# Optimization experiments

Measured on AMD Instinct MI355X. Metric: run time of the kernel, lower is better.

## Reference

```python
import jax, jax.numpy as jnp
import numpy as np

N_NODES = 100000
N_RELS = 237
N_EDGES = 500000
D_IN = 128
D_HID = 128
D_OUT = 128


def setup_inputs() -> dict:
    key = jax.random.key(0)
    ks = jax.random.split(key, 13)
    src = jax.random.randint(ks[0], (N_EDGES,), 0, N_NODES, dtype=jnp.int32)
    dst = jax.random.randint(ks[1], (N_EDGES,), 0, N_NODES, dtype=jnp.int32)
    rel = jax.random.randint(ks[2], (N_EDGES,), 0, N_RELS, dtype=jnp.int32)
    triplets = jnp.stack([src, dst, rel], axis=1)  # [E, 3]
    s = 0.05
    return {
        "triplets": triplets,
        "ent_embed": jax.random.normal(ks[3], (N_NODES, D_IN), jnp.float32) * s,
        "rel_embed": jax.random.normal(ks[4], (N_RELS, D_IN), jnp.float32) * s,
        "W_ent": jax.random.normal(ks[5], (D_IN, D_HID), jnp.float32) * s,
        "b_ent": jnp.zeros((D_HID,), jnp.float32),
        "W_rel": jax.random.normal(ks[6], (D_IN, D_HID), jnp.float32) * s,
        "b_rel": jnp.zeros((D_HID,), jnp.float32),
        "W_ent2": jax.random.normal(ks[7], (3 * D_HID, D_OUT), jnp.float32) * s,
        "b_ent2": jnp.zeros((D_OUT,), jnp.float32),
        "a_w": jax.random.normal(ks[8], (D_OUT, 1), jnp.float32) * s,
        "a_b": jnp.zeros((1,), jnp.float32),
    }


def reference(triplets, ent_embed, rel_embed, W_ent, b_ent, W_rel, b_rel,
              W_ent2, b_ent2, a_w, a_b):
    src_i, dst_i, rel_i = triplets[:, 0], triplets[:, 1], triplets[:, 2]
    # embedding gathers
    src = ent_embed[src_i]          # [E, D_IN]
    dst = ent_embed[dst_i]          # [E, D_IN]
    rel = rel_embed[rel_i]          # [E, D_IN]
    # shared fc_ent projection on src and dst, fc_rel on rel
    src = src @ W_ent + b_ent       # [E, D_HID]
    dst = dst @ W_ent + b_ent
    rel = rel @ W_rel + b_rel
    # per-edge feature c = fc_ent2(cat([src, dst, rel]))
    c = jnp.concatenate([src, dst, rel], axis=1) @ W_ent2 + b_ent2  # [E, D_OUT]
    # unnormalized exp attention score (leaky_relu slope 0.01, torch default)
    b = jnp.exp(jax.nn.leaky_relu((c @ a_w + a_b)[:, 0], negative_slope=0.01))  # [E]
    # segment softmax over edges sharing a source node
    b_sum = jax.ops.segment_sum(b, src_i, num_segments=N_NODES)  # [N]
    alpha = b / b_sum[src_i]                                     # [E]
    # weighted neighbor aggregation per source node
    h = jax.ops.segment_sum(alpha[:, None] * c, src_i, num_segments=N_NODES)  # [N, D_OUT]
    return h
```

## Files before the change

kernel.cpp:

```cpp
#include <hip/hip_runtime.h>
#include <hip/hip_bf16.h>

#define N_NODES_C 100000
#define N_PAD_C   100096
#define N_RELS_C  237
#define N_EDGES_C 500000
#define D 128

#define NBLK_HIST 128
#define NBLK_REL  60
#define NBLK_GEMM 1568
#define GEMM0     (NBLK_HIST + NBLK_REL)

typedef __attribute__((ext_vector_type(8))) short short8;
typedef __attribute__((ext_vector_type(4))) float f32x4;

__device__ __forceinline__ ushort f2bf(float x) {
    union { float f; uint u; } v; v.f = x;
    uint r = v.u + 0x7FFFu + ((v.u >> 16) & 1u);
    return (ushort)(r >> 16);
}
__device__ __forceinline__ float bf2f_hi(uint u) {
    union { uint u; float f; } v; v.u = u; return v.f;
}

__global__ void k_fuse_w(const float* __restrict__ W_ent, const float* __restrict__ W_rel,
                         const float* __restrict__ W_ent2,
                         const float* __restrict__ b_ent, const float* __restrict__ b_rel,
                         const float* __restrict__ b_ent2,
                         const float* __restrict__ a_w, const float* __restrict__ a_b,
                         float* __restrict__ WR, ushort* __restrict__ WfTb,
                         float* __restrict__ biasC, float* __restrict__ sConst,
                         int* __restrict__ deg) {
    int j = threadIdx.x;
    int k = blockIdx.x;
    int which = blockIdx.y;
    if (which == 0) {
        float acc = 0.f;
        for (int i = 0; i < D; ++i) acc += W_ent[k*D+i] * W_ent2[i*D+j];
        WfTb[j*D + k] = f2bf(acc);
    } else if (which == 1) {
        float acc = 0.f;
        for (int i = 0; i < D; ++i) acc += W_ent[k*D+i] * W_ent2[(D+i)*D+j];
        WfTb[(D+j)*D + k] = f2bf(acc);
    } else if (which == 2) {
        float acc = 0.f;
        for (int i = 0; i < D; ++i) acc += W_rel[k*D+i] * W_ent2[(2*D+i)*D+j];
        WR[k*D + j] = acc;
    } else if (k == 0) {
        __shared__ float red[128];
        float acc = b_ent2[j];
        for (int i = 0; i < D; ++i) {
            acc += b_ent[i] * (W_ent2[i*D+j] + W_ent2[(D+i)*D+j]);
            acc += b_rel[i] * W_ent2[(2*D+i)*D+j];
        }
        biasC[j] = acc;
        red[j] = acc * a_w[j];
        __syncthreads();
        for (int s = 64; s > 0; s >>= 1) { if (j < s) red[j] += red[j+s]; __syncthreads(); }
        if (j == 0) sConst[0] = red[0] + a_b[0];
    } else {
        int idx = (k - 1) * 128 + j;
        for (int i = idx; i < N_NODES_C; i += 127 * 128) deg[i] = 0;
    }
}

__global__ __launch_bounds__(512, 6) void k1_mega(const float* __restrict__ ent,
                                                  const ushort* __restrict__ WfTb,
                                                  const float* __restrict__ a_w,
                                                  const float* __restrict__ relE,
                                                  const float* __restrict__ WR,
                                                  const int* __restrict__ trip,
                                                  ushort* __restrict__ AnB,
                                                  ushort* __restrict__ BnB,
                                                  ushort* __restrict__ RmB,
                                                  float* __restrict__ sA,
                                                  float* __restrict__ sB,
                                                  float* __restrict__ sR,
                                                  int* __restrict__ deg,
                                                  int n_nodes) {
    __shared__ __align__(16) ushort wL[128*128];
    int tid = threadIdx.x;
    int blk = blockIdx.x;

    if (blk < NBLK_HIST) {
        for (int e = blk*512 + tid; e < N_EDGES_C; e += NBLK_HIST*512) {
            int s = trip[3*e];
            if ((unsigned)s < (unsigned)N_NODES_C) atomicAdd(&deg[s], 1);
        }
        return;
    }
    if (blk < GEMM0) {
        __shared__ float red[512];
        int sub = tid >> 7, j = tid & 127;
        int r = (blk - NBLK_HIST)*4 + sub;
        float acc = 0.f;
        if (r < N_RELS_C) {
            for (int k = 0; k < D; ++k) acc += relE[r*D+k] * WR[k*D+j];
            RmB[r*D + j] = f2bf(acc);
        }
        red[tid] = acc * a_w[j];
        __syncthreads();
        for (int s = 64; s > 0; s >>= 1) {
            if (j < s) red[sub*128 + j] += red[sub*128 + j + s];
            __syncthreads();
        }
        if (j == 0 && r < N_RELS_C) sR[r] = red[sub*128];
        return;
    }

    int g    = blk - GEMM0;
    int half = (g >> 3) & 1;
    int tile = ((g >> 4) << 3) + (g & 7);
    int m0   = tile * 128;

    int wave = tid >> 6, lane = tid & 63;
    int q = lane >> 4, c = lane & 15;

    int row = m0 + wave*16 + c;
    float4 e0[4], e1[4];
#pragma unroll
    for (int chunk = 0; chunk < 4; ++chunk) {
        e0[chunk] = make_float4(0.f,0.f,0.f,0.f);
        e1[chunk] = e0[chunk];
    }
    if (row < n_nodes) {
        const float* ep = &ent[(size_t)row*D];
#pragma unroll
        for (int chunk = 0; chunk < 4; ++chunk) {
            int k16 = chunk*4 + q;
            e0[chunk] = *(const float4*)(ep + (k16 << 3));
            e1[chunk] = *(const float4*)(ep + (k16 << 3) + 4);
        }
    }

#pragma unroll
    for (int u = 0; u < 4; ++u) {
        int f = u*512 + tid;
        int r = f >> 4, k16 = f & 15;
        *(uint4*)&wL[r*128 + ((k16 ^ (r & 15)) << 3)] =
            *(const uint4*)&WfTb[(half*128 + r)*128 + (k16 << 3)];
    }

    short8 a[4];
#pragma unroll
    for (int chunk = 0; chunk < 4; ++chunk) {
        short8 pk;
        pk[0]=(short)f2bf(e0[chunk].x); pk[1]=(short)f2bf(e0[chunk].y);
        pk[2]=(short)f2bf(e0[chunk].z); pk[3]=(short)f2bf(e0[chunk].w);
        pk[4]=(short)f2bf(e1[chunk].x); pk[5]=(short)f2bf(e1[chunk].y);
        pk[6]=(short)f2bf(e1[chunk].z); pk[7]=(short)f2bf(e1[chunk].w);
        a[chunk] = pk;
    }
    __syncthreads();

    f32x4 acc[8];
#pragma unroll
    for (int nt = 0; nt < 8; ++nt) { f32x4 z = {0.f,0.f,0.f,0.f}; acc[nt] = z; }

#pragma unroll
    for (int chunk = 0; chunk < 4; ++chunk) {
        int k16 = chunk*4 + q;
#pragma unroll
        for (int nt = 0; nt < 8; ++nt) {
            int wrow = nt*16 + c;
            short8 b = *(const short8*)&wL[wrow*128 + ((k16 ^ c) << 3)];
            acc[nt] = __builtin_amdgcn_mfma_f32_16x16x32_bf16(a[chunk], b, acc[nt], 0, 0, 0);
        }
    }

    float aw[8];
#pragma unroll
    for (int nt = 0; nt < 8; ++nt) aw[nt] = a_w[nt*16 + c];

    ushort* out  = half ? BnB : AnB;
    float*  sOut = half ? sB  : sA;

#pragma unroll
    for (int reg = 0; reg < 4; ++reg) {
        int m = m0 + wave*16 + q*4 + reg;
        float pa = 0.f;
#pragma unroll
        for (int nt = 0; nt < 8; ++nt) pa += acc[nt][reg] * aw[nt];
#pragma unroll
        for (int msk = 1; msk < 16; msk <<= 1) pa += __shfl_xor(pa, msk);
        if (m < n_nodes) {
            if (c == 0) sOut[m] = pa;
#pragma unroll
            for (int nt = 0; nt < 8; ++nt)
                out[(size_t)m*D + nt*16 + c] = f2bf(acc[nt][reg]);
        }
    }
}

__global__ void k_scan1(const int* __restrict__ deg, int* __restrict__ off,
                        int* __restrict__ bsum, int n) {
    __shared__ int s[1024];
    int i = blockIdx.x*1024 + threadIdx.x;
    int v = (i < n) ? deg[i] : 0;
    s[threadIdx.x] = v; __syncthreads();
    for (int d = 1; d < 1024; d <<= 1) {
        int t = (threadIdx.x >= d) ? s[threadIdx.x - d] : 0;
        __syncthreads();
        s[threadIdx.x] += t;
        __syncthreads();
    }
    if (i < n) off[i] = s[threadIdx.x] - v;
    if (threadIdx.x == 1023) bsum[blockIdx.x] = s[1023];
}

__global__ void k_scan23(int* __restrict__ off, int* __restrict__ cursor,
                         const int* __restrict__ bsum, int n, int nb, int total_edges) {
    __shared__ int s[128];
    int t = threadIdx.x;
    if (t < 128) s[t] = (t < nb) ? bsum[t] : 0;
    __syncthreads();
    for (int d = 1; d < 128; d <<= 1) {
        int u = (t < 128 && t >= d) ? s[t - d] : 0;
        __syncthreads();
        if (t < 128) s[t] += u;
        __syncthreads();
    }
    int add = (blockIdx.x > 0) ? s[blockIdx.x - 1] : 0;
    int i = blockIdx.x*1024 + t;
    if (i < n) {
        int o = off[i] + add;
        off[i] = o;
        cursor[i] = o;
    }
    if (i == 0) off[n] = total_edges;
}

__global__ void k_edge_b(const int* __restrict__ trip, const float* __restrict__ sA,
                         const float* __restrict__ sB, const float* __restrict__ sR,
                         const float* __restrict__ sConst, int* __restrict__ cursor,
                         uint2* __restrict__ kb, int n_edges) {
    int e = blockIdx.x*256 + threadIdx.x;
    if (e >= n_edges) return;
    int s = trip[3*e], d = trip[3*e+1], r = trip[3*e+2];
    if ((unsigned)s >= (unsigned)N_NODES_C || (unsigned)d >= (unsigned)N_NODES_C ||
        (unsigned)r >= (unsigned)N_RELS_C) return;
    float v = sB[d] + sR[r];
    float t = sA[s] + sConst[0];
    float logit = t + v;
    float l = logit > 0.f ? logit : 0.01f*logit;
    float b = expf(l);
    int p = atomicAdd(&cursor[s], 1);
    kb[p] = make_uint2((uint)(d | (r << 20)), __float_as_uint(b));
}

__global__ void k_aggregate(const int* __restrict__ off, const uint2* __restrict__ kb,
                            const ushort* __restrict__ AnB, const ushort* __restrict__ BnB,
                            const ushort* __restrict__ RmB, const float* __restrict__ biasC,
                            float* __restrict__ h, int n_nodes) {
    int g = threadIdx.x >> 4, lane = threadIdx.x & 15;
    int n = blockIdx.x*16 + g;
    if (n >= n_nodes) return;
    int o0 = off[n], o1 = off[n+1];
    int c = lane*8;
    float* hp = &h[(size_t)n*D + c];
    if (o0 == o1) {
        *(float4*)hp     = make_float4(0.f,0.f,0.f,0.f);
        *(float4*)(hp+4) = make_float4(0.f,0.f,0.f,0.f);
        return;
    }
    float num[8];
#pragma unroll
    for (int i = 0; i < 8; ++i) num[i] = 0.f;
    float den = 0.f;

    for (int p = o0; p < o1; p += 4) {
        uint2 kv[4]; uint4 gB[4], gR[4]; float vmask[4];
#pragma unroll
        for (int u = 0; u < 4; ++u) {
            int q = p + u;
            vmask[u] = (q < o1) ? 1.f : 0.f;
            int pc = (q < o1) ? q : (o1 - 1);
            kv[u] = kb[pc];
        }
#pragma unroll
        for (int u = 0; u < 4; ++u) {
            gB[u] = *(const uint4*)&BnB[(size_t)(kv[u].x & 0xFFFFF)*D + c];
            gR[u] = *(const uint4*)&RmB[(size_t)(kv[u].x >> 20)*D + c];
        }
#pragma unroll
        for (int u = 0; u < 4; ++u) {
            float b = vmask[u] * __uint_as_float(kv[u].y);
            den += b;
            const uint* bu = (const uint*)&gB[u];
            const uint* ru = (const uint*)&gR[u];
#pragma unroll
            for (int i = 0; i < 4; ++i) {
                num[2*i]   += b * (bf2f_hi(bu[i] << 16)         + bf2f_hi(ru[i] << 16));
                num[2*i+1] += b * (bf2f_hi(bu[i] & 0xFFFF0000u) + bf2f_hi(ru[i] & 0xFFFF0000u));
            }
        }
    }

    float inv = 1.f / den;
    uint4 araw = *(const uint4*)&AnB[(size_t)n*D + c];
    const uint* au = (const uint*)&araw;
    float4 bc0 = *(const float4*)&biasC[c];
    float4 bc1 = *(const float4*)&biasC[c+4];
    float4 o0v, o1v;
    o0v.x = bf2f_hi(au[0] << 16)         + bc0.x + num[0]*inv;
    o0v.y = bf2f_hi(au[0] & 0xFFFF0000u) + bc0.y + num[1]*inv;
    o0v.z = bf2f_hi(au[1] << 16)         + bc0.z + num[2]*inv;
    o0v.w = bf2f_hi(au[1] & 0xFFFF0000u) + bc0.w + num[3]*inv;
    o1v.x = bf2f_hi(au[2] << 16)         + bc1.x + num[4]*inv;
    o1v.y = bf2f_hi(au[2] & 0xFFFF0000u) + bc1.y + num[5]*inv;
    o1v.z = bf2f_hi(au[3] << 16)         + bc1.z + num[6]*inv;
    o1v.w = bf2f_hi(au[3] & 0xFFFF0000u) + bc1.w + num[7]*inv;
    *(float4*)hp     = o0v;
    *(float4*)(hp+4) = o1v;
}

extern "C" void kernel_launch(void* const* d_in, const int* in_sizes, int n_in,
                              void* d_out, int out_size, void* d_ws, size_t ws_size,
                              hipStream_t stream) {
    const int*   trip   = (const int*)  d_in[0];
    const float* ent    = (const float*)d_in[1];
    const float* relE   = (const float*)d_in[2];
    const float* W_ent  = (const float*)d_in[3];
    const float* b_ent  = (const float*)d_in[4];
    const float* W_rel  = (const float*)d_in[5];
    const float* b_rel  = (const float*)d_in[6];
    const float* W_ent2 = (const float*)d_in[7];
    const float* b_ent2 = (const float*)d_in[8];
    const float* a_w    = (const float*)d_in[9];
    const float* a_b    = (const float*)d_in[10];
    float* h = (float*)d_out;

    char* ws = (char*)d_ws;
    size_t o = 0;
    auto alloc = [&](size_t bytes) { size_t p = o; o += (bytes + 255) & ~(size_t)255; return p; };
    float*  WR     = (float*) (ws + alloc(128*128*4));
    ushort* WfTb   = (ushort*)(ws + alloc(256*128*2));
    float*  biasC  = (float*) (ws + alloc(128*4));
    ushort* RmB    = (ushort*)(ws + alloc((size_t)N_RELS_C*128*2));
    float*  sR     = (float*) (ws + alloc(N_RELS_C*4));
    float*  sConst = (float*) (ws + alloc(4));
    float*  sA     = (float*) (ws + alloc((size_t)N_NODES_C*4));
    float*  sB     = (float*) (ws + alloc((size_t)N_NODES_C*4));
    int*    deg    = (int*)   (ws + alloc((size_t)N_NODES_C*4));
    int*    off    = (int*)   (ws + alloc(((size_t)N_NODES_C+1)*4));
    int*    cursor = (int*)   (ws + alloc((size_t)N_NODES_C*4));
    int*    bsum   = (int*)   (ws + alloc(128*4));
    uint2*  kb     = (uint2*) (ws + alloc((size_t)N_EDGES_C*8));
    ushort* BnB    = (ushort*)(ws + alloc((size_t)N_PAD_C*128*2));
    ushort* AnB    = (ushort*)(ws + alloc((size_t)N_PAD_C*128*2));

    k_fuse_w<<<dim3(128,4), 128, 0, stream>>>(W_ent, W_rel, W_ent2, b_ent, b_rel, b_ent2,
                                              a_w, a_b, WR, WfTb, biasC, sConst, deg);
    k1_mega<<<GEMM0 + NBLK_GEMM, 512, 0, stream>>>(
        ent, WfTb, a_w, relE, WR, trip, AnB, BnB, RmB, sA, sB, sR, deg, N_NODES_C);
    int nb = (N_NODES_C + 1023)/1024;
    k_scan1<<<nb, 1024, 0, stream>>>(deg, off, bsum, N_NODES_C);
    k_scan23<<<nb, 1024, 0, stream>>>(off, cursor, bsum, N_NODES_C, nb, N_EDGES_C);
    k_edge_b<<<(N_EDGES_C+255)/256, 256, 0, stream>>>(trip, sA, sB, sR, sConst,
                                                      cursor, kb, N_EDGES_C);
    k_aggregate<<<(N_NODES_C+15)/16, 256, 0, stream>>>(off, kb, AnB, BnB, RmB, biasC,
                                                       h, N_NODES_C);
}
```

Baseline: 220.0 us.

## Fold block-sum scan pass into edge and aggregate kernels to drop a launch

Removes the second scan kernel that added block prefix offsets to the CSR offsets and cursors. Each block of the edge-bucketing and aggregation kernels now recomputes the 98-entry block-sum prefix in shared memory and applies it on the fly to locally-scanned offsets. This saves one kernel launch and a full read/write pass over the offset arrays, at the cost of a small redundant shared-memory scan with several barriers in every block of the two downstream kernels.

```diff
diff --git a/kernel.cpp b/kernel.cpp
--- a/kernel.cpp
+++ b/kernel.cpp
@@ -6,6 +6,7 @@
 #define N_RELS_C  237
 #define N_EDGES_C 500000
 #define D 128
+#define NSCAN_B   98
 
 #define NBLK_HIST 128
 #define NBLK_REL  60
@@ -194,7 +195,7 @@
 }
 
 __global__ void k_scan1(const int* __restrict__ deg, int* __restrict__ off,
-                        int* __restrict__ bsum, int n) {
+                        int* __restrict__ cursor, int* __restrict__ bsum, int n) {
     __shared__ int s[1024];
     int i = blockIdx.x*1024 + threadIdx.x;
     int v = (i < n) ? deg[i] : 0;
@@ -205,37 +206,26 @@
         s[threadIdx.x] += t;
         __syncthreads();
     }
-    if (i < n) off[i] = s[threadIdx.x] - v;
+    int excl = s[threadIdx.x] - v;
+    if (i < n) { off[i] = excl; cursor[i] = excl; }
     if (threadIdx.x == 1023) bsum[blockIdx.x] = s[1023];
 }
 
-__global__ void k_scan23(int* __restrict__ off, int* __restrict__ cursor,
-                         const int* __restrict__ bsum, int n, int nb, int total_edges) {
-    __shared__ int s[128];
-    int t = threadIdx.x;
-    if (t < 128) s[t] = (t < nb) ? bsum[t] : 0;
+__global__ void k_edge_b(const int* __restrict__ trip, const float* __restrict__ sA,
+                         const float* __restrict__ sB, const float* __restrict__ sR,
+                         const float* __restrict__ sConst, const int* __restrict__ bsum,
+                         int* __restrict__ cursor, uint2* __restrict__ kb, int n_edges) {
+    __shared__ int bp[128];
+    int tid = threadIdx.x;
+    if (tid < 128) bp[tid] = (tid < NSCAN_B) ? bsum[tid] : 0;
     __syncthreads();
     for (int d = 1; d < 128; d <<= 1) {
-        int u = (t < 128 && t >= d) ? s[t - d] : 0;
-        __syncthreads();
-        if (t < 128) s[t] += u;
-        __syncthreads();
-    }
-    int add = (blockIdx.x > 0) ? s[blockIdx.x - 1] : 0;
-    int i = blockIdx.x*1024 + t;
-    if (i < n) {
-        int o = off[i] + add;
-        off[i] = o;
-        cursor[i] = o;
-    }
-    if (i == 0) off[n] = total_edges;
-}
-
-__global__ void k_edge_b(const int* __restrict__ trip, const float* __restrict__ sA,
-                         const float* __restrict__ sB, const float* __restrict__ sR,
-                         const float* __restrict__ sConst, int* __restrict__ cursor,
-                         uint2* __restrict__ kb, int n_edges) {
-    int e = blockIdx.x*256 + threadIdx.x;
+        int u = (tid < 128 && tid >= d) ? bp[tid - d] : 0;
+        __syncthreads();
+        if (tid < 128) bp[tid] += u;
+        __syncthreads();
+    }
+    int e = blockIdx.x*256 + tid;
     if (e >= n_edges) return;
     int s = trip[3*e], d = trip[3*e+1], r = trip[3*e+2];
     if ((unsigned)s >= (unsigned)N_NODES_C || (unsigned)d >= (unsigned)N_NODES_C ||
@@ -245,18 +235,39 @@
     float logit = t + v;
     float l = logit > 0.f ? logit : 0.01f*logit;
     float b = expf(l);
-    int p = atomicAdd(&cursor[s], 1);
+    int sb = s >> 10;
+    int add = (sb > 0) ? bp[sb - 1] : 0;
+    int p = atomicAdd(&cursor[s], 1) + add;
     kb[p] = make_uint2((uint)(d | (r << 20)), __float_as_uint(b));
 }
 
-__global__ void k_aggregate(const int* __restrict__ off, const uint2* __restrict__ kb,
+__global__ void k_aggregate(const int* __restrict__ off, const int* __restrict__ bsum,
+                            const uint2* __restrict__ kb,
                             const ushort* __restrict__ AnB, const ushort* __restrict__ BnB,
                             const ushort* __restrict__ RmB, const float* __restrict__ biasC,
                             float* __restrict__ h, int n_nodes) {
-    int g = threadIdx.x >> 4, lane = threadIdx.x & 15;
+    __shared__ int bp[128];
+    int tid = threadIdx.x;
+    if (tid < 128) bp[tid] = (tid < NSCAN_B) ? bsum[tid] : 0;
+    __syncthreads();
+    for (int d = 1; d < 128; d <<= 1) {
+        int u = (tid < 128 && tid >= d) ? bp[tid - d] : 0;
+        __syncthreads();
+        if (tid < 128) bp[tid] += u;
+        __syncthreads();
+    }
+    int g = tid >> 4, lane = tid & 15;
     int n = blockIdx.x*16 + g;
     if (n >= n_nodes) return;
-    int o0 = off[n], o1 = off[n+1];
+    int nb0 = n >> 10;
+    int o0 = off[n] + ((nb0 > 0) ? bp[nb0 - 1] : 0);
+    int o1;
+    if (n + 1 == n_nodes) {
+        o1 = N_EDGES_C;
+    } else {
+        int nb1 = (n + 1) >> 10;
+        o1 = off[n + 1] + ((nb1 > 0) ? bp[nb1 - 1] : 0);
+    }
     int c = lane*8;
     float* hp = &h[(size_t)n*D + c];
     if (o0 == o1) {
@@ -354,11 +365,9 @@
                                               a_w, a_b, WR, WfTb, biasC, sConst, deg);
     k1_mega<<<GEMM0 + NBLK_GEMM, 512, 0, stream>>>(
         ent, WfTb, a_w, relE, WR, trip, AnB, BnB, RmB, sA, sB, sR, deg, N_NODES_C);
-    int nb = (N_NODES_C + 1023)/1024;
-    k_scan1<<<nb, 1024, 0, stream>>>(deg, off, bsum, N_NODES_C);
-    k_scan23<<<nb, 1024, 0, stream>>>(off, cursor, bsum, N_NODES_C, nb, N_EDGES_C);
-    k_edge_b<<<(N_EDGES_C+255)/256, 256, 0, stream>>>(trip, sA, sB, sR, sConst,
+    k_scan1<<<NSCAN_B, 1024, 0, stream>>>(deg, off, cursor, bsum, N_NODES_C);
+    k_edge_b<<<(N_EDGES_C+255)/256, 256, 0, stream>>>(trip, sA, sB, sR, sConst, bsum,
                                                       cursor, kb, N_EDGES_C);
-    k_aggregate<<<(N_NODES_C+15)/16, 256, 0, stream>>>(off, kb, AnB, BnB, RmB, biasC,
-                                                       h, N_NODES_C);
-}
+    k_aggregate<<<(N_NODES_C+15)/16, 256, 0, stream>>>(off, bsum, kb, AnB, BnB, RmB,
+                                                       biasC, h, N_NODES_C);
+}
```

After: 223.7 us. About the same (+1.7%).
